# Performance work log

Measured on AMD Instinct MI355X. Metric: run time of the kernel, lower is better.

## Reference

```python
import jax, jax.numpy as jnp
import numpy as np

THETA = 100000.0

def _rope(x, pos, theta=THETA):
    # x: [..., H, S, d_k]; pos: [S] int
    d_k = x.shape[-1]
    half = d_k // 2
    inv_freq = theta ** (-(jnp.arange(half, dtype=jnp.float32) / half))  # theta^{-2i/d}
    ang = pos.astype(jnp.float32)[:, None] * inv_freq[None, :]  # [S, half]
    cos, sin = jnp.cos(ang), jnp.sin(ang)
    x1 = x[..., 0::2]
    x2 = x[..., 1::2]
    r1 = x1 * cos - x2 * sin
    r2 = x1 * sin + x2 * cos
    # interleave back to [..., d_k]
    return jnp.stack([r1, r2], axis=-1).reshape(x.shape)


def setup_inputs() -> dict:
    key = jax.random.key(0)
    ks = jax.random.split(key, 5)
    B, S, D = 1, 4096, 1024
    x = jax.random.normal(ks[0], (B, S, D), dtype=jnp.float32)
    sc = 1.0 / np.sqrt(D)
    Wq = jax.random.normal(ks[1], (D, D), dtype=jnp.float32) * sc
    Wk = jax.random.normal(ks[2], (D, D), dtype=jnp.float32) * sc
    Wv = jax.random.normal(ks[3], (D, D), dtype=jnp.float32) * sc
    Wo = jax.random.normal(ks[4], (D, D), dtype=jnp.float32) * sc
    token_positions = jnp.arange(S, dtype=jnp.int32)
    return {"x": x, "Wq": Wq, "Wk": Wk, "Wv": Wv, "Wo": Wo, "token_positions": token_positions}


def reference(x, Wq, Wk, Wv, Wo, token_positions):
    H = 16
    B, S, D = x.shape
    d_k = D // H
    # Linear (no bias): y = x @ W^T
    Q = jnp.einsum('bsd,ed->bse', x, Wq)
    K = jnp.einsum('bsd,ed->bse', x, Wk)
    V = jnp.einsum('bsd,ed->bse', x, Wv)
    # [B, H, S, d_k]
    Q = Q.reshape(B, S, H, d_k).transpose(0, 2, 1, 3)
    K = K.reshape(B, S, H, d_k).transpose(0, 2, 1, 3)
    V = V.reshape(B, S, H, d_k).transpose(0, 2, 1, 3)
    Q = _rope(Q, token_positions)
    K = _rope(K, token_positions)
    scores = jnp.einsum('bhqd,bhkd->bhqk', Q, K) / jnp.sqrt(jnp.float32(d_k))
    causal = jnp.tril(jnp.ones((S, S), dtype=bool))
    scores = jnp.where(causal, scores, jnp.finfo(scores.dtype).min)
    probs = jax.nn.softmax(scores, axis=-1)
    attn = jnp.einsum('bhqk,bhkd->bhqd', probs, V)
    attn = attn.transpose(0, 2, 1, 3).reshape(B, S, D)
    return jnp.einsum('bsd,ed->bse', attn, Wo)
```

## Files before the change

kernel.cpp:

```cpp
#include <hip/hip_runtime.h>

typedef float f32x4 __attribute__((ext_vector_type(4)));
typedef short s16x8 __attribute__((ext_vector_type(8)));
typedef int   i32x2 __attribute__((ext_vector_type(2)));
typedef int   i32x4 __attribute__((ext_vector_type(4)));

#define DEV static __device__ __forceinline__

DEV short f2bf(float f) {
    unsigned u = __builtin_bit_cast(unsigned, f);
    u += 0x7FFFu + ((u >> 16) & 1u);
    return (short)(u >> 16);
}
DEV float bf2f(short s) {
    return __builtin_bit_cast(float, ((unsigned)(unsigned short)s) << 16);
}
DEV int cvtpk(float lo, float hi) {
    int r;
    asm("v_cvt_pk_bf16_f32 %0, %1, %2" : "=v"(r) : "v"(lo), "v"(hi));
    return r;
}
DEV float fexp2(float x) { float r; asm("v_exp_f32 %0, %1" : "=v"(r) : "v"(x)); return r; }
DEV float ffract(float x){ float r; asm("v_fract_f32 %0, %1" : "=v"(r) : "v"(x)); return r; }
DEV float fsin(float x)  { float r; asm("v_sin_f32 %0, %1" : "=v"(r) : "v"(x)); return r; }
DEV float fcos(float x)  { float r; asm("v_cos_f32 %0, %1" : "=v"(r) : "v"(x)); return r; }
DEV f32x4 mfma_bf16(s16x8 a, s16x8 b, f32x4 c) {
    asm("v_mfma_f32_16x16x32_bf16 %0, %1, %2, %0" : "+v"(c) : "v"(a), "v"(b));
    return c;
}
DEV f32x4 mfma16_bf16(i32x2 a, i32x2 b, f32x4 c) {
    asm("v_mfma_f32_16x16x16_bf16 %0, %1, %2, %0" : "+v"(c) : "v"(a), "v"(b));
    return c;
}
DEV void gl_lds16(const void* g, void* l) {
    __builtin_amdgcn_global_load_lds((const __attribute__((address_space(1))) unsigned*)g,
                                     (__attribute__((address_space(3))) unsigned*)l, 16, 0, 0);
}

__global__ __launch_bounds__(256) void conv_kernel(
    const float* __restrict__ x,
    const float* __restrict__ W0, const float* __restrict__ W1,
    const float* __restrict__ W2, const float* __restrict__ W3,
    short* __restrict__ xb,
    short* __restrict__ B0, short* __restrict__ B1,
    short* __restrict__ B2, short* __restrict__ B3)
{
    const int bid = blockIdx.x, tid = threadIdx.x;
    const float* src;
    short* dst;
    size_t off;
    if (bid < 2048) {
        src = x; dst = xb; off = (size_t)bid * 2048 + tid * 8;
    } else {
        int t = bid - 2048, wi = t >> 9;
        src = wi == 0 ? W0 : (wi == 1 ? W1 : (wi == 2 ? W2 : W3));
        dst = wi == 0 ? B0 : (wi == 1 ? B1 : (wi == 2 ? B2 : B3));
        off = (size_t)(t & 511) * 2048 + tid * 8;
    }
    f32x4 v0 = *(const f32x4*)(src + off);
    f32x4 v1 = *(const f32x4*)(src + off + 4);
    s16x8 o;
    #pragma unroll
    for (int e = 0; e < 4; e++) { o[e] = f2bf(v0[e]); o[4 + e] = f2bf(v1[e]); }
    *(s16x8*)(dst + off) = o;
}

template<int BM, int OUT_BF16, int ROPE>
__global__ __launch_bounds__(256) void gemm128(
    const short* __restrict__ A,
    const short* __restrict__ Bq, const short* __restrict__ Bk, const short* __restrict__ Bv,
    void* __restrict__ Cq, void* __restrict__ Ck, void* __restrict__ Cv,
    const int* __restrict__ posp)
{
    constexpr int KD = 1024, ND = 1024;
    constexpr int MI = BM / 32;
    __shared__ __align__(16) short As[BM * 32];
    __shared__ __align__(16) short Bs[128 * 32];
    const int n0 = blockIdx.x * 128, m0 = blockIdx.y * BM;
    const int zz = blockIdx.z;
    const short* B = zz == 0 ? Bq : (zz == 1 ? Bk : Bv);
    void* C       = zz == 0 ? Cq : (zz == 1 ? Ck : Cv);
    const int tid = threadIdx.x;
    const int lane = tid & 63, w = tid >> 6, g = lane >> 4, c = lane & 15;
    const int wm = w >> 1, wn = w & 1;

    const int swz = (tid & 3) ^ ((tid >> 3) & 3);
    const short* a0 = A + (size_t)(m0 + (tid >> 2)) * KD + 8 * swz;
    const short* a1 = a0 + (size_t)64 * KD;
    const short* b0 = B + (size_t)(n0 + (tid >> 2)) * KD + 8 * swz;
    const short* b1 = b0 + (size_t)64 * KD;
    char* ldsA = (char*)As + w * 1024;
    char* ldsB = (char*)Bs + w * 1024;

    int aoff[MI], boff[4];
    #pragma unroll
    for (int i = 0; i < MI; i++) {
        int ar = wm * (BM / 2) + i * 16 + c;
        aoff[i] = ar * 64 + (g ^ ((ar >> 1) & 3)) * 16;
    }
    #pragma unroll
    for (int j = 0; j < 4; j++) {
        int br = wn * 64 + j * 16 + c;
        boff[j] = br * 64 + (g ^ ((br >> 1) & 3)) * 16;
    }

    f32x4 acc[MI][4] = {};

    for (int k0 = 0; k0 < KD; k0 += 32) {
        __syncthreads();
        gl_lds16(a0 + k0, ldsA);
        if (BM == 128) gl_lds16(a1 + k0, ldsA + 4096);
        gl_lds16(b0 + k0, ldsB);
        gl_lds16(b1 + k0, ldsB + 4096);
        __syncthreads();
        s16x8 af[MI], bf[4];
        #pragma unroll
        for (int i = 0; i < MI; i++) af[i] = *(const s16x8*)((const char*)As + aoff[i]);
        #pragma unroll
        for (int j = 0; j < 4; j++) bf[j] = *(const s16x8*)((const char*)Bs + boff[j]);
        #pragma unroll
        for (int i = 0; i < MI; i++)
            #pragma unroll
            for (int j = 0; j < 4; j++)
                acc[i][j] = mfma_bf16(af[i], bf[j], acc[i][j]);
    }

    if (ROPE && zz <= 1) {
        const float ps = (zz == 0) ? 0.18033688011112042f : 1.0f;
        #pragma unroll
        for (int j = 0; j < 4; j++) {
            int col = n0 + wn * 64 + j * 16 + c;
            float invf = fexp2(-(float)((col & 63) >> 1) * 0.51905126482615036f)
                       * 0.15915494309189535f;
            float ssign = (col & 1) ? 1.f : -1.f;
            #pragma unroll
            for (int i = 0; i < MI; i++)
                #pragma unroll
                for (int r = 0; r < 4; r++) {
                    int row = m0 + wm * (BM / 2) + i * 16 + 4 * g + r;
                    float fp = (float)posp[row];
                    float fr = ffract(fp * invf);
                    float sn = fsin(fr) * ps, cs = fcos(fr) * ps;
                    float own = acc[i][j][r];
                    float oth = __shfl_xor(own, 1);
                    acc[i][j][r] = own * cs + oth * (ssign * sn);
                }
        }
    }

    #pragma unroll
    for (int i = 0; i < MI; i++)
        #pragma unroll
        for (int j = 0; j < 4; j++)
            #pragma unroll
            for (int r = 0; r < 4; r++) {
                int row = m0 + wm * (BM / 2) + i * 16 + 4 * g + r;
                int col = n0 + wn * 64 + j * 16 + c;
                float v = acc[i][j][r];
                if (OUT_BF16) ((short*)C)[(size_t)row * ND + col] = f2bf(v);
                else          ((float*)C)[(size_t)row * ND + col] = v;
            }
}

template<int A_BF16, int OUT_BF16>
__global__ __launch_bounds__(256) void gemm_bt(
    const void* __restrict__ Ap,
    const float* __restrict__ B0, const float* __restrict__ B1, const float* __restrict__ B2,
    void* __restrict__ C0, void* __restrict__ C1, void* __restrict__ C2)
{
    constexpr int KD = 1024, ND = 1024;
    __shared__ short As[64][40];
    __shared__ short Bs[64][40];
    const int n0 = blockIdx.x * 64, m0 = blockIdx.y * 64;
    const float* Bw = blockIdx.z == 0 ? B0 : (blockIdx.z == 1 ? B1 : B2);
    void* Cw       = blockIdx.z == 0 ? C0 : (blockIdx.z == 1 ? C1 : C2);
    const int tid = threadIdx.x;
    const int lane = tid & 63, w = tid >> 6, g = lane >> 4, c = lane & 15;
    const int wm = w >> 1, wn = w & 1;
    const int sr = tid >> 2, scc = (tid & 3) * 8;

    f32x4 acc[2][2] = {};

    for (int k0 = 0; k0 < KD; k0 += 32) {
        __syncthreads();
        if (A_BF16) {
            *(s16x8*)&As[sr][scc] =
                *(const s16x8*)((const short*)Ap + (size_t)(m0 + sr) * KD + k0 + scc);
        } else {
            const float* ap = (const float*)Ap + (size_t)(m0 + sr) * KD + k0 + scc;
            f32x4 va = *(const f32x4*)ap, vb = *(const f32x4*)(ap + 4);
            s16x8 av;
            #pragma unroll
            for (int e = 0; e < 4; e++) { av[e] = f2bf(va[e]); av[4 + e] = f2bf(vb[e]); }
            *(s16x8*)&As[sr][scc] = av;
        }
        {
            const float* bp = Bw + (size_t)(n0 + sr) * KD + k0 + scc;
            f32x4 va = *(const f32x4*)bp, vb = *(const f32x4*)(bp + 4);
            s16x8 bv;
            #pragma unroll
            for (int e = 0; e < 4; e++) { bv[e] = f2bf(va[e]); bv[4 + e] = f2bf(vb[e]); }
            *(s16x8*)&Bs[sr][scc] = bv;
        }
        __syncthreads();
        s16x8 af[2], bfv[2];
        #pragma unroll
        for (int i = 0; i < 2; i++) af[i]  = *(const s16x8*)&As[wm * 32 + i * 16 + c][8 * g];
        #pragma unroll
        for (int j = 0; j < 2; j++) bfv[j] = *(const s16x8*)&Bs[wn * 32 + j * 16 + c][8 * g];
        #pragma unroll
        for (int i = 0; i < 2; i++)
            #pragma unroll
            for (int j = 0; j < 2; j++)
                acc[i][j] = mfma_bf16(af[i], bfv[j], acc[i][j]);
    }

    #pragma unroll
    for (int i = 0; i < 2; i++)
        #pragma unroll
        for (int j = 0; j < 2; j++)
            #pragma unroll
            for (int r = 0; r < 4; r++) {
                int row = m0 + wm * 32 + i * 16 + 4 * g + r;
                int col = n0 + wn * 32 + j * 16 + c;
                float v = acc[i][j][r];
                if (OUT_BF16) ((short*)Cw)[(size_t)row * ND + col] = f2bf(v);
                else          ((float*)Cw)[(size_t)row * ND + col] = v;
            }
}

__global__ __launch_bounds__(256) void rope_kernel(short* Q, short* K, const int* __restrict__ posp)
{
    const int t = blockIdx.x * 256 + threadIdx.x;
    const int isK = blockIdx.y;
    short* ptr = isK ? K : Q;
    const float postscale = isK ? 1.0f : 0.18033688011112042f;
    const int idx  = t * 8;
    const int srow = idx >> 10;
    const int dd   = (idx & 1023) & 63;
    const int p0   = dd >> 1;
    const float fp = (float)posp[srow];
    s16x8 v = *(s16x8*)(ptr + idx);
    s16x8 o;
    #pragma unroll
    for (int pr = 0; pr < 4; pr++) {
        float ex  = fexp2(-(float)(p0 + pr) * 0.51905126482615036f);
        float ang = fp * ex * 0.15915494309189535f;
        float fr  = ffract(ang);
        float sn  = fsin(fr) * postscale;
        float cs  = fcos(fr) * postscale;
        float x1 = bf2f(v[2 * pr]), x2 = bf2f(v[2 * pr + 1]);
        o[2 * pr]     = f2bf(x1 * cs - x2 * sn);
        o[2 * pr + 1] = f2bf(x1 * sn + x2 * cs);
    }
    *(s16x8*)(ptr + idx) = o;
}

template<int NZ>
__global__ __launch_bounds__(256, 3) void attn_kernel(
    const short* __restrict__ Q, const short* __restrict__ K,
    const short* __restrict__ V, short* __restrict__ O0,
    short* __restrict__ O1, short* __restrict__ O2, short* __restrict__ O3,
    float* __restrict__ Lf)
{
    constexpr int D = 1024;
    int qx, h, z;
    if (NZ > 1) {
        const int B = blockIdx.x;
        const int xcd = B & 7, k = B >> 3;
        h = xcd + 8 * (k / (16 * NZ));
        const int r = k % (16 * NZ);
        qx = r & 15;
        z = r >> 4;
    } else {
        qx = blockIdx.x; h = blockIdx.y; z = 0;
    }
    const int hc = h * 64;
    short* O = (z == 0) ? O0 : (z == 1 ? O1 : (z == 2 ? O2 : O3));
    const int tid = threadIdx.x;
    const int w = tid >> 6, lane = tid & 63, g = lane >> 4, c = lane & 15;

    __shared__ __align__(16) int Kl[2][64 * 32];
    __shared__ __align__(16) int Vl[2][64][32];

    const int krow_l = lane >> 3;
    const int kchunk = (lane & 7) ^ krow_l;
    const short* Kpre = K + hc + (size_t)(w * 16 + krow_l) * D + kchunk * 8;
    char* kdst0 = (char*)&Kl[0][0] + w * 16 * 128;
    char* kdst1 = (char*)&Kl[1][0] + w * 16 * 128;

    const int vkvp = tid & 31;
    const int vd0 = (tid >> 5) * 8;
    const short* Vpre = V + hc + (size_t)(2 * vkvp) * D + vd0;

    int koff0[4], koff1[4];
    #pragma unroll
    for (int t = 0; t < 4; t++) {
        int row = t * 16 + c;
        koff0[t] = row * 128 + ((g) ^ (row & 7)) * 16;
        koff1[t] = row * 128 + ((4 + g) ^ (row & 7)) * 16;
    }

    for (int pi = 0; pi < 2; pi++) {
        const int qq = pi ? 31 - qx : qx;
        const int wqb = qq * 128 + w * 32;
        s16x8 bq[2][2];
        #pragma unroll
        for (int m = 0; m < 2; m++) {
            const short* qp = Q + (size_t)(wqb + m * 16 + c) * D + hc + 8 * g;
            bq[m][0] = *(const s16x8*)qp;
            bq[m][1] = *(const s16x8*)(qp + 32);
        }

        f32x4 acc[2][4] = {};
        float l2[2] = {0.f, 0.f};
        const int nkb = 2 * qq + 2;

        __syncthreads();
        s16x8 vs0, vs1;
        {
            gl_lds16(Kpre + (size_t)(z * 64) * D, kdst0);
            gl_lds16(Kpre + (size_t)(z * 64 + 8) * D, kdst0 + 8 * 128);
            const short* vp = Vpre + (size_t)(z * 64) * D;
            vs0 = *(const s16x8*)vp;
            vs1 = *(const s16x8*)(vp + D);
        }

        int cur = 0;
        for (int kb = z; kb < nkb; kb += NZ, cur ^= 1) {
            #pragma unroll
            for (int e = 0; e < 8; e++) {
                unsigned dw = (unsigned)(unsigned short)vs0[e] | ((unsigned)(unsigned short)vs1[e] << 16);
                Vl[cur][vd0 + e][vkvp ^ (4 * e)] = (int)dw;
            }
            asm volatile("s_waitcnt vmcnt(0)" ::: "memory");
            __syncthreads();

            const bool more = (kb + NZ) < nkb;
            if (more) {
                const int kb1 = kb + NZ;
                char* kd = cur ? kdst0 : kdst1;
                gl_lds16(Kpre + (size_t)(kb1 * 64) * D, kd);
                gl_lds16(Kpre + (size_t)(kb1 * 64 + 8) * D, kd + 8 * 128);
                const short* vp = Vpre + (size_t)(kb1 * 64) * D;
                vs0 = *(const s16x8*)vp;
                vs1 = *(const s16x8*)(vp + D);
            }

            if (kb * 64 > wqb + 31) continue;

            const char* Kb = (const char*)&Kl[cur][0];
            f32x4 st[2][4];
            __builtin_amdgcn_s_setprio(1);
            #pragma unroll
            for (int t = 0; t < 4; t++) {
                s16x8 a0 = *(const s16x8*)(Kb + koff0[t]);
                s16x8 a1 = *(const s16x8*)(Kb + koff1[t]);
                f32x4 z0 = {};
                z0 = mfma_bf16(a0, bq[0][0], z0);
                z0 = mfma_bf16(a1, bq[0][1], z0);
                st[0][t] = z0;
                f32x4 z1 = {};
                z1 = mfma_bf16(a0, bq[1][0], z1);
                z1 = mfma_bf16(a1, bq[1][1], z1);
                st[1][t] = z1;
            }
            __builtin_amdgcn_s_setprio(0);

            i32x2 pd[2][4];
            #pragma unroll
            for (int m = 0; m < 2; m++) {
                const int wqm = wqb + m * 16;
                const int qrow = wqm + c;
                float p[16];
                if (kb * 64 + 63 > wqm) {
                    #pragma unroll
                    for (int t = 0; t < 4; t++)
                        #pragma unroll
                        for (int i = 0; i < 4; i++) {
                            int kv = kb * 64 + t * 16 + 4 * g + i;
                            float e = fexp2(st[m][t][i]);
                            if (kv > qrow) e = 0.f;
                            p[t * 4 + i] = e;
                            l2[m] += e;
                        }
                } else {
                    #pragma unroll
                    for (int t = 0; t < 4; t++)
                        #pragma unroll
                        for (int i = 0; i < 4; i++) {
                            float e = fexp2(st[m][t][i]);
                            p[t * 4 + i] = e;
                            l2[m] += e;
                        }
                }
                #pragma unroll
                for (int t = 0; t < 4; t++) {
                    pd[m][t][0] = cvtpk(p[t * 4 + 0], p[t * 4 + 1]);
                    pd[m][t][1] = cvtpk(p[t * 4 + 2], p[t * 4 + 3]);
                }
            }

            __builtin_amdgcn_s_setprio(1);
            #pragma unroll
            for (int t = 0; t < 4; t++) {
                #pragma unroll
                for (int jt = 0; jt < 4; jt++) {
                    i32x2 vb = *(const i32x2*)&Vl[cur][jt * 16 + c][(t * 8 + 2 * g) ^ (4 * (c & 7))];
                    acc[0][jt] = mfma16_bf16(pd[0][t], vb, acc[0][jt]);
                    acc[1][jt] = mfma16_bf16(pd[1][t], vb, acc[1][jt]);
                }
            }
            __builtin_amdgcn_s_setprio(0);
        }

        #pragma unroll
        for (int m = 0; m < 2; m++) {
            float lsum = l2[m] + __shfl_xor(l2[m], 16);
            lsum += __shfl_xor(lsum, 32);
            if (NZ > 1 && lane < 16) {
                float Lv = (lsum > 0.f) ? __log2f(lsum) : -1e30f;
                Lf[(size_t)(z * 16 + h) * 4096 + (wqb + m * 16 + lane)] = Lv;
            }
            float linv[4];
            #pragma unroll
            for (int i = 0; i < 4; i++) {
                float ls = __shfl(lsum, 4 * g + i);
                linv[i] = (ls > 0.f) ? 1.f / ls : 0.f;
            }
            #pragma unroll
            for (int jt = 0; jt < 4; jt++)
                #pragma unroll
                for (int i = 0; i < 4; i++) {
                    int r = wqb + m * 16 + 4 * g + i;
                    O[(size_t)r * D + hc + jt * 16 + c] = f2bf(acc[m][jt][i] * linv[i]);
                }
        }
    }
}

template<int NP>
__global__ __launch_bounds__(256) void combine_kernel(
    short* __restrict__ Aw, const short* __restrict__ P1,
    const short* __restrict__ P2, const short* __restrict__ P3,
    const float* __restrict__ Lf)
{
    const int t = blockIdx.x * 256 + threadIdx.x;
    const int idx = t * 8;
    const int row = idx >> 10, col = idx & 1023, h = col >> 6;
    float L[NP];
    float LM = -1e30f;
    #pragma unroll
    for (int zi = 0; zi < NP; zi++) {
        L[zi] = Lf[(size_t)(zi * 16 + h) * 4096 + row];
        LM = fmaxf(LM, L[zi]);
    }
    float wz[NP], wsum = 0.f;
    #pragma unroll
    for (int zi = 0; zi < NP; zi++) { wz[zi] = fexp2(L[zi] - LM); wsum += wz[zi]; }
    float inv = 1.f / wsum;
    #pragma unroll
    for (int zi = 0; zi < NP; zi++) wz[zi] *= inv;

    const short* Ps[4] = {Aw, P1, P2, P3};
    f32x4 o0 = {}, o1 = {};
    #pragma unroll
    for (int zi = 0; zi < NP; zi++) {
        s16x8 a = *(const s16x8*)(Ps[zi] + idx);
        #pragma unroll
        for (int e = 0; e < 4; e++) o0[e] += wz[zi] * bf2f(a[e]);
        #pragma unroll
        for (int e = 0; e < 4; e++) o1[e] += wz[zi] * bf2f(a[4 + e]);
    }
    s16x8 o;
    #pragma unroll
    for (int e = 0; e < 4; e++) { o[e] = f2bf(o0[e]); o[4 + e] = f2bf(o1[e]); }
    *(s16x8*)(Aw + idx) = o;
}

extern "C" void kernel_launch(void* const* d_in, const int* in_sizes, int n_in,
                              void* d_out, int out_size, void* d_ws, size_t ws_size,
                              hipStream_t stream)
{
    const float* x  = (const float*)d_in[0];
    const float* Wq = (const float*)d_in[1];
    const float* Wk = (const float*)d_in[2];
    const float* Wv = (const float*)d_in[3];
    const float* Wo = (const float*)d_in[4];
    const int*  pos = (const int*)d_in[5];
    float* out = (float*)d_out;

    const size_t SD = (size_t)4096 * 1024;
    const size_t WSZ = (size_t)1024 * 1024;
    short* Qw = (short*)d_ws;
    short* Kw = Qw + SD;
    short* Vw = Kw + SD;
    short* Aw = Vw + SD;

    const size_t need_A4 = (7 * SD + 4 * WSZ) * sizeof(short) + 4 * 16 * 4096 * sizeof(float);
    const size_t need_A2 = (5 * SD + 4 * WSZ) * sizeof(short) + 2 * 16 * 4096 * sizeof(float);
    const size_t need_B  = (4 * SD + 4 * WSZ) * sizeof(short);

    if (ws_size >= need_A4) {
        short* P1  = Aw + SD;
        short* P2  = P1 + SD;
        short* P3  = P2 + SD;
        short* xb  = Aw;
        short* Wqb = P3 + SD;
        short* Wkb = Wqb + WSZ;
        short* Wvb = Wkb + WSZ;
        short* Wob = Wvb + WSZ;
        float* Lf  = (float*)(Wob + WSZ);
        conv_kernel<<<4096, 256, 0, stream>>>(x, Wq, Wk, Wv, Wo, xb, Wqb, Wkb, Wvb, Wob);
        gemm128<128, 1, 1><<<dim3(8, 32, 3), 256, 0, stream>>>(xb, Wqb, Wkb, Wvb, Qw, Kw, Vw, pos);
        attn_kernel<4><<<1024, 256, 0, stream>>>(Qw, Kw, Vw, Aw, P1, P2, P3, Lf);
        combine_kernel<4><<<2048, 256, 0, stream>>>(Aw, P1, P2, P3, Lf);
        gemm128<64, 0, 0><<<dim3(8, 64, 1), 256, 0, stream>>>(Aw, Wob, Wob, Wob, out, out, out, pos);
    } else if (ws_size >= need_A2) {
        short* P1  = Aw + SD;
        short* xb  = Aw;
        short* Wqb = P1 + SD;
        short* Wkb = Wqb + WSZ;
        short* Wvb = Wkb + WSZ;
        short* Wob = Wvb + WSZ;
        float* Lf  = (float*)(Wob + WSZ);
        conv_kernel<<<4096, 256, 0, stream>>>(x, Wq, Wk, Wv, Wo, xb, Wqb, Wkb, Wvb, Wob);
        gemm128<128, 1, 1><<<dim3(8, 32, 3), 256, 0, stream>>>(xb, Wqb, Wkb, Wvb, Qw, Kw, Vw, pos);
        attn_kernel<2><<<512, 256, 0, stream>>>(Qw, Kw, Vw, Aw, P1, P1, P1, Lf);
        combine_kernel<2><<<2048, 256, 0, stream>>>(Aw, P1, P1, P1, Lf);
        gemm128<64, 0, 0><<<dim3(8, 64, 1), 256, 0, stream>>>(Aw, Wob, Wob, Wob, out, out, out, pos);
    } else if (ws_size >= need_B) {
        short* xb  = Aw;
        short* Wqb = Aw + SD;
        short* Wkb = Wqb + WSZ;
        short* Wvb = Wkb + WSZ;
        short* Wob = Wvb + WSZ;
        conv_kernel<<<4096, 256, 0, stream>>>(x, Wq, Wk, Wv, Wo, xb, Wqb, Wkb, Wvb, Wob);
        gemm128<128, 1, 1><<<dim3(8, 32, 3), 256, 0, stream>>>(xb, Wqb, Wkb, Wvb, Qw, Kw, Vw, pos);
        attn_kernel<1><<<dim3(16, 16, 1), 256, 0, stream>>>(Qw, Kw, Vw, Aw, Aw, Aw, Aw, nullptr);
        gemm128<64, 0, 0><<<dim3(8, 64, 1), 256, 0, stream>>>(Aw, Wob, Wob, Wob, out, out, out, pos);
    } else {
        gemm_bt<0, 1><<<dim3(16, 64, 3), 256, 0, stream>>>(x, Wq, Wk, Wv, Qw, Kw, Vw);
        rope_kernel<<<dim3(2048, 2), 256, 0, stream>>>(Qw, Kw, pos);
        attn_kernel<1><<<dim3(16, 16, 1), 256, 0, stream>>>(Qw, Kw, Vw, Aw, Aw, Aw, Aw, nullptr);
        gemm_bt<1, 0><<<dim3(16, 64, 1), 256, 0, stream>>>(Aw, Wo, Wo, Wo, out, out, out);
    }
}
```

Before: 134.3 us.

## Fuse split-KV partial combine into output projection GEMM A-tile load

Removes the separate combine kernel and instead merges the attention partials (weighted by log-sum-exp factors) inside the Wo GEMM while loading each A tile. The combined bf16 values are written directly to LDS. This avoids one kernel launch plus writing and re-reading the combined activation. The cost is that each of the 8 column blocks recomputes the combine, reading 4 partial buffers and the LSE values. The synchronous load path also replaces the async global-to-LDS copy, which may stall the k-loop.

```diff
diff --git a/kernel.cpp b/kernel.cpp
--- a/kernel.cpp
+++ b/kernel.cpp
@@ -65,12 +65,14 @@
     *(s16x8*)(dst + off) = o;
 }
 
-template<int BM, int OUT_BF16, int ROPE>
+template<int BM, int OUT_BF16, int ROPE, int NP>
 __global__ __launch_bounds__(256) void gemm128(
     const short* __restrict__ A,
     const short* __restrict__ Bq, const short* __restrict__ Bk, const short* __restrict__ Bv,
     void* __restrict__ Cq, void* __restrict__ Ck, void* __restrict__ Cv,
-    const int* __restrict__ posp)
+    const int* __restrict__ posp,
+    const short* __restrict__ PA1, const short* __restrict__ PA2,
+    const short* __restrict__ PA3, const float* __restrict__ Lf)
 {
     constexpr int KD = 1024, ND = 1024;
     constexpr int MI = BM / 32;
@@ -85,7 +87,8 @@
     const int wm = w >> 1, wn = w & 1;
 
     const int swz = (tid & 3) ^ ((tid >> 3) & 3);
-    const short* a0 = A + (size_t)(m0 + (tid >> 2)) * KD + 8 * swz;
+    const size_t aoff_g = (size_t)(m0 + (tid >> 2)) * KD + 8 * swz;
+    const short* a0 = A + aoff_g;
     const short* a1 = a0 + (size_t)64 * KD;
     const short* b0 = B + (size_t)(n0 + (tid >> 2)) * KD + 8 * swz;
     const short* b1 = b0 + (size_t)64 * KD;
@@ -108,8 +111,38 @@
 
     for (int k0 = 0; k0 < KD; k0 += 32) {
         __syncthreads();
-        gl_lds16(a0 + k0, ldsA);
-        if (BM == 128) gl_lds16(a1 + k0, ldsA + 4096);
+        if (NP == 0) {
+            gl_lds16(a0 + k0, ldsA);
+            if (BM == 128) gl_lds16(a1 + k0, ldsA + 4096);
+        } else {
+            const int kk = k0 + 8 * swz;
+            const int head = kk >> 6;
+            const int arow = m0 + (tid >> 2);
+            float L[NP > 0 ? NP : 1];
+            float LM = -1e30f;
+            #pragma unroll
+            for (int zi = 0; zi < NP; zi++) {
+                L[zi] = Lf[(size_t)(zi * 16 + head) * 4096 + arow];
+                LM = fmaxf(LM, L[zi]);
+            }
+            float wz[NP > 0 ? NP : 1], ws = 0.f;
+            #pragma unroll
+            for (int zi = 0; zi < NP; zi++) { wz[zi] = fexp2(L[zi] - LM); ws += wz[zi]; }
+            float inv = 1.f / ws;
+            const short* Pp[4] = {A, PA1, PA2, PA3};
+            float o8[8] = {};
+            #pragma unroll
+            for (int zi = 0; zi < NP; zi++) {
+                s16x8 v = *(const s16x8*)(Pp[zi] + aoff_g + k0);
+                float wzi = wz[zi] * inv;
+                #pragma unroll
+                for (int e = 0; e < 8; e++) o8[e] += wzi * bf2f(v[e]);
+            }
+            s16x8 ov;
+            #pragma unroll
+            for (int e = 0; e < 8; e++) ov[e] = f2bf(o8[e]);
+            *(s16x8*)(ldsA + (size_t)lane * 16) = ov;
+        }
         gl_lds16(b0 + k0, ldsB);
         gl_lds16(b1 + k0, ldsB + 4096);
         __syncthreads();
@@ -439,45 +472,6 @@
     }
 }
 
-template<int NP>
-__global__ __launch_bounds__(256) void combine_kernel(
-    short* __restrict__ Aw, const short* __restrict__ P1,
-    const short* __restrict__ P2, const short* __restrict__ P3,
-    const float* __restrict__ Lf)
-{
-    const int t = blockIdx.x * 256 + threadIdx.x;
-    const int idx = t * 8;
-    const int row = idx >> 10, col = idx & 1023, h = col >> 6;
-    float L[NP];
-    float LM = -1e30f;
-    #pragma unroll
-    for (int zi = 0; zi < NP; zi++) {
-        L[zi] = Lf[(size_t)(zi * 16 + h) * 4096 + row];
-        LM = fmaxf(LM, L[zi]);
-    }
-    float wz[NP], wsum = 0.f;
-    #pragma unroll
-    for (int zi = 0; zi < NP; zi++) { wz[zi] = fexp2(L[zi] - LM); wsum += wz[zi]; }
-    float inv = 1.f / wsum;
-    #pragma unroll
-    for (int zi = 0; zi < NP; zi++) wz[zi] *= inv;
-
-    const short* Ps[4] = {Aw, P1, P2, P3};
-    f32x4 o0 = {}, o1 = {};
-    #pragma unroll
-    for (int zi = 0; zi < NP; zi++) {
-        s16x8 a = *(const s16x8*)(Ps[zi] + idx);
-        #pragma unroll
-        for (int e = 0; e < 4; e++) o0[e] += wz[zi] * bf2f(a[e]);
-        #pragma unroll
-        for (int e = 0; e < 4; e++) o1[e] += wz[zi] * bf2f(a[4 + e]);
-    }
-    s16x8 o;
-    #pragma unroll
-    for (int e = 0; e < 4; e++) { o[e] = f2bf(o0[e]); o[4 + e] = f2bf(o1[e]); }
-    *(s16x8*)(Aw + idx) = o;
-}
-
 extern "C" void kernel_launch(void* const* d_in, const int* in_sizes, int n_in,
                               void* d_out, int out_size, void* d_ws, size_t ws_size,
                               hipStream_t stream)
@@ -512,10 +506,11 @@
         short* Wob = Wvb + WSZ;
         float* Lf  = (float*)(Wob + WSZ);
         conv_kernel<<<4096, 256, 0, stream>>>(x, Wq, Wk, Wv, Wo, xb, Wqb, Wkb, Wvb, Wob);
-        gemm128<128, 1, 1><<<dim3(8, 32, 3), 256, 0, stream>>>(xb, Wqb, Wkb, Wvb, Qw, Kw, Vw, pos);
+        gemm128<128, 1, 1, 0><<<dim3(8, 32, 3), 256, 0, stream>>>(
+            xb, Wqb, Wkb, Wvb, Qw, Kw, Vw, pos, nullptr, nullptr, nullptr, nullptr);
         attn_kernel<4><<<1024, 256, 0, stream>>>(Qw, Kw, Vw, Aw, P1, P2, P3, Lf);
-        combine_kernel<4><<<2048, 256, 0, stream>>>(Aw, P1, P2, P3, Lf);
-        gemm128<64, 0, 0><<<dim3(8, 64, 1), 256, 0, stream>>>(Aw, Wob, Wob, Wob, out, out, out, pos);
+        gemm128<64, 0, 0, 4><<<dim3(8, 64, 1), 256, 0, stream>>>(
+            Aw, Wob, Wob, Wob, out, out, out, pos, P1, P2, P3, Lf);
     } else if (ws_size >= need_A2) {
         short* P1  = Aw + SD;
         short* xb  = Aw;
@@ -525,10 +520,11 @@
         short* Wob = Wvb + WSZ;
         float* Lf  = (float*)(Wob + WSZ);
         conv_kernel<<<4096, 256, 0, stream>>>(x, Wq, Wk, Wv, Wo, xb, Wqb, Wkb, Wvb, Wob);
-        gemm128<128, 1, 1><<<dim3(8, 32, 3), 256, 0, stream>>>(xb, Wqb, Wkb, Wvb, Qw, Kw, Vw, pos);
+        gemm128<128, 1, 1, 0><<<dim3(8, 32, 3), 256, 0, stream>>>(
+            xb, Wqb, Wkb, Wvb, Qw, Kw, Vw, pos, nullptr, nullptr, nullptr, nullptr);
         attn_kernel<2><<<512, 256, 0, stream>>>(Qw, Kw, Vw, Aw, P1, P1, P1, Lf);
-        combine_kernel<2><<<2048, 256, 0, stream>>>(Aw, P1, P1, P1, Lf);
-        gemm128<64, 0, 0><<<dim3(8, 64, 1), 256, 0, stream>>>(Aw, Wob, Wob, Wob, out, out, out, pos);
+        gemm128<64, 0, 0, 2><<<dim3(8, 64, 1), 256, 0, stream>>>(
+            Aw, Wob, Wob, Wob, out, out, out, pos, P1, P1, P1, Lf);
     } else if (ws_size >= need_B) {
         short* xb  = Aw;
         short* Wqb = Aw + SD;
@@ -536,9 +532,11 @@
         short* Wvb = Wkb + WSZ;
         short* Wob = Wvb + WSZ;
         conv_kernel<<<4096, 256, 0, stream>>>(x, Wq, Wk, Wv, Wo, xb, Wqb, Wkb, Wvb, Wob);
-        gemm128<128, 1, 1><<<dim3(8, 32, 3), 256, 0, stream>>>(xb, Wqb, Wkb, Wvb, Qw, Kw, Vw, pos);
+        gemm128<128, 1, 1, 0><<<dim3(8, 32, 3), 256, 0, stream>>>(
+            xb, Wqb, Wkb, Wvb, Qw, Kw, Vw, pos, nullptr, nullptr, nullptr, nullptr);
         attn_kernel<1><<<dim3(16, 16, 1), 256, 0, stream>>>(Qw, Kw, Vw, Aw, Aw, Aw, Aw, nullptr);
-        gemm128<64, 0, 0><<<dim3(8, 64, 1), 256, 0, stream>>>(Aw, Wob, Wob, Wob, out, out, out, pos);
+        gemm128<64, 0, 0, 0><<<dim3(8, 64, 1), 256, 0, stream>>>(
+            Aw, Wob, Wob, Wob, out, out, out, pos, nullptr, nullptr, nullptr, nullptr);
     } else {
         gemm_bt<0, 1><<<dim3(16, 64, 3), 256, 0, stream>>>(x, Wq, Wk, Wv, Qw, Kw, Vw);
         rope_kernel<<<dim3(2048, 2), 256, 0, stream>>>(Qw, Kw, pos);
```

Result: slower. 154.0 us (+14.7%).
